# Optimization experiments

Hardware: AMD Instinct MI355X
Metric: run time of the kernel (lower is better)

The kernel has to match this reference:

```python
import jax, jax.numpy as jnp
import numpy as np

# Module config (matches init_kwargs)
C = 256          # in_channels
H = 8            # num_heads
T, L = 32, 16    # partition_size
S = T * L        # tokens per window = 512
B_ = 64          # number of windows
SCALE = H ** (-0.5)  # faithful to source: num_heads**-0.5


def setup_inputs() -> dict:
    key = jax.random.key(0)
    ks = jax.random.split(key, 6)
    x = jax.random.normal(ks[0], (B_, S, C), dtype=jnp.float32)
    # nn.Linear(C, 3C) weights: [out, in], bias: [out]
    qkv_w = jax.random.normal(ks[1], (3 * C, C), dtype=jnp.float32) * (1.0 / np.sqrt(C))
    qkv_b = jnp.zeros((3 * C,), dtype=jnp.float32)
    proj_w = jax.random.normal(ks[2], (C, C), dtype=jnp.float32) * (1.0 / np.sqrt(C))
    proj_b = jnp.zeros((C,), dtype=jnp.float32)
    # relative_position_bias_table for type_2: (2T-1, L, L, H), trunc_normal std=0.02 ~ small normal
    rel_table = jax.random.normal(ks[3], (2 * T - 1, L, L, H), dtype=jnp.float32) * 0.02
    return {"x": x, "qkv_w": qkv_w, "qkv_b": qkv_b,
            "proj_w": proj_w, "proj_b": proj_b, "rel_table": rel_table}


def _relative_position_bias(rel_table):
    # 1D relative index over T temporal positions, values in [0, 2T-2]
    idx = jnp.arange(T)[:, None] - jnp.arange(T)[None, :] + (T - 1)  # [T, T]
    b = rel_table[idx]                        # [T, T, L, L, H]
    b = b.transpose(0, 2, 1, 3, 4)            # [T, L, T, L, H]
    b = b.reshape(S, S, H)                    # [S, S, H]
    return b.transpose(2, 0, 1)[None]         # [1, H, S, S]


def reference(x, qkv_w, qkv_b, proj_w, proj_b, rel_table):
    Bw, Sw, Cw = x.shape
    d = Cw // H
    qkv = x @ qkv_w.T + qkv_b                              # [B_, S, 3C]
    qkv = qkv.reshape(Bw, Sw, 3, H, d).transpose(2, 0, 3, 1, 4)  # [3, B_, H, S, d]
    q, k, v = qkv[0], qkv[1], qkv[2]
    attn = jnp.einsum('bhsd,bhtd->bhst', q * SCALE, k)     # [B_, H, S, S]
    attn = attn + _relative_position_bias(rel_table)
    attn = jax.nn.softmax(attn, axis=-1)
    # attn_drop p=0.0 -> identity
    out = jnp.einsum('bhst,bhtd->bhsd', attn, v)           # [B_, H, S, d]
    out = out.transpose(0, 2, 1, 3).reshape(Bw, Sw, Cw)    # [B_, S, C]
    out = out @ proj_w.T + proj_b
    # proj_drop p=0.0 -> identity
    return out
```

## Files before the change

### kernel.cpp

```cpp
#include <hip/hip_runtime.h>
#include <stdint.h>

#define NB 64
#define NS 512
#define NC 256
#define NH 8
#define ND 32

typedef __attribute__((ext_vector_type(8))) short s8v;
typedef __attribute__((ext_vector_type(8))) unsigned short u8v;
typedef __attribute__((ext_vector_type(4))) float f4v;

#define LOG2E 1.4426950408889634f

static __device__ __forceinline__ uint16_t f2bf(float f) {
    uint32_t u = __builtin_bit_cast(uint32_t, f);
    u += 0x7fffu + ((u >> 16) & 1u);
    return (uint16_t)(u >> 16);
}
static __device__ __forceinline__ float bf2f(uint16_t h) {
    uint32_t u = ((uint32_t)h) << 16;
    return __builtin_bit_cast(float, u);
}
static __device__ __forceinline__ uint32_t cvtpk(float lo, float hi) {
    uint32_t r;
    asm("v_cvt_pk_bf16_f32 %0, %1, %2" : "=v"(r) : "v"(lo), "v"(hi));
    return r;
}

#if __has_builtin(__builtin_amdgcn_permlane32_swap)
static __device__ __forceinline__ void pl32(uint32_t& a, uint32_t& b) {
    auto r = __builtin_amdgcn_permlane32_swap(a, b, false, false);
    a = r[0]; b = r[1];
}
static __device__ __forceinline__ void pl16(uint32_t& a, uint32_t& b) {
    auto r = __builtin_amdgcn_permlane16_swap(a, b, false, false);
    a = r[0]; b = r[1];
}
#else
static __device__ __forceinline__ void pl32(uint32_t& a, uint32_t& b) {
    asm volatile("v_permlane32_swap_b32 %0, %1" : "+v"(a), "+v"(b));
}
static __device__ __forceinline__ void pl16(uint32_t& a, uint32_t& b) {
    asm volatile("v_permlane16_swap_b32 %0, %1" : "+v"(a), "+v"(b));
}
#endif

__global__ __launch_bounds__(256) void cvt_all(const float* __restrict__ x,
                                               const float* __restrict__ wq,
                                               const float* __restrict__ wp,
                                               uint16_t* __restrict__ xo,
                                               uint16_t* __restrict__ wqo,
                                               uint16_t* __restrict__ wpo) {
    int i = (blockIdx.x * 256 + threadIdx.x) * 8;
    const float* src; uint16_t* dst; int off;
    if (i < 8388608)      { src = x;  dst = xo;  off = i; }
    else if (i < 8585216) { src = wq; dst = wqo; off = i - 8388608; }
    else                  { src = wp; dst = wpo; off = i - 8585216; }
    f4v a = *(const f4v*)(src + off);
    f4v b = *(const f4v*)(src + off + 4);
    uint4 w;
    w.x = cvtpk(a[0], a[1]); w.y = cvtpk(a[2], a[3]);
    w.z = cvtpk(b[0], b[1]); w.w = cvtpk(b[2], b[3]);
    *(uint4*)(dst + off) = w;
}

__global__ __launch_bounds__(256) void rel_fill(const float* __restrict__ rel,
                                                uint16_t* __restrict__ rel2) {
    int id = blockIdx.x * 256 + threadIdx.x;
    int h = id / 20480, rem = id % 20480;
    int dt = rem / 320, q = rem % 320;
    int li = q / 20, lj = q % 20;
    float v = (lj < 16 && dt < 63) ? rel[(((dt << 4) + li) * 16 + lj) * 8 + h] * LOG2E : 0.f;
    rel2[id] = f2bf(v);
}

__global__ __launch_bounds__(256) void qkv_gemm(const uint16_t* __restrict__ X,
                                                const uint16_t* __restrict__ W,
                                                const float* __restrict__ Bv,
                                                uint16_t* __restrict__ Qo,
                                                uint16_t* __restrict__ Ko,
                                                uint16_t* __restrict__ Vo) {
    __shared__ uint16_t As[2][128 * 40];
    __shared__ uint16_t Bs[2][128 * 40];
    const int tid = threadIdx.x;
    const int bn = blockIdx.y * 128;
    const int bm = blockIdx.x * 128;
    const int lane = tid & 63, wv = tid >> 6;
    const int wm = (wv >> 1) * 64, wn = (wv & 1) * 64;
    const int lq = lane & 15, g = lane >> 4;
    const int srow = tid >> 1;
    const int scol = (tid & 1) * 16;

    const uint16_t* xs = X + (size_t)(bm + srow) * 256 + scol;
    const uint16_t* wsrc = W + (size_t)(bn + srow) * 256 + scol;

    f4v acc[4][4] = {};
    u8v xa, xb, wa, wb;

    xa = *(const u8v*)(xs);     xb = *(const u8v*)(xs + 8);
    wa = *(const u8v*)(wsrc);   wb = *(const u8v*)(wsrc + 8);
    *(u8v*)(&As[0][srow * 40 + scol])     = xa;
    *(u8v*)(&As[0][srow * 40 + scol + 8]) = xb;
    *(u8v*)(&Bs[0][srow * 40 + scol])     = wa;
    *(u8v*)(&Bs[0][srow * 40 + scol + 8]) = wb;
    __syncthreads();

    for (int ks = 0; ks < 8; ++ks) {
        const int cur = ks & 1;
        if (ks < 7) {
            const int k1 = (ks + 1) * 32;
            xa = *(const u8v*)(xs + k1);   xb = *(const u8v*)(xs + k1 + 8);
            wa = *(const u8v*)(wsrc + k1); wb = *(const u8v*)(wsrc + k1 + 8);
        }
        s8v af[4], bf[4];
        #pragma unroll
        for (int i = 0; i < 4; ++i) {
            af[i] = *(const s8v*)(&As[cur][(wm + i * 16 + lq) * 40 + g * 8]);
            bf[i] = *(const s8v*)(&Bs[cur][(wn + i * 16 + lq) * 40 + g * 8]);
        }
        #pragma unroll
        for (int mt = 0; mt < 4; ++mt)
            #pragma unroll
            for (int nt = 0; nt < 4; ++nt)
                acc[mt][nt] = __builtin_amdgcn_mfma_f32_16x16x32_bf16(af[mt], bf[nt], acc[mt][nt], 0, 0, 0);
        if (ks < 7) {
            *(u8v*)(&As[cur ^ 1][srow * 40 + scol])     = xa;
            *(u8v*)(&As[cur ^ 1][srow * 40 + scol + 8]) = xb;
            *(u8v*)(&Bs[cur ^ 1][srow * 40 + scol])     = wa;
            *(u8v*)(&Bs[cur ^ 1][srow * 40 + scol + 8]) = wb;
        }
        __syncthreads();
    }

    const int gsel = bn >> 8;
    const float scl = (gsel == 0) ? (0.35355339059327373f * LOG2E) : 1.0f;
    #pragma unroll
    for (int nt = 0; nt < 4; ++nt) {
        const int ng = bn + wn + nt * 16 + lq;
        const float bv = Bv[ng];
        const int c = ng & 255, hh = c >> 5, dd = c & 31;
        #pragma unroll
        for (int mt = 0; mt < 4; ++mt) {
            #pragma unroll
            for (int r = 0; r < 4; ++r) {
                const int m = bm + wm + mt * 16 + g * 4 + r;
                const int b = m >> 9, s = m & 511;
                const uint16_t val = f2bf((acc[mt][nt][r] + bv) * scl);
                if (gsel == 0)      Qo[((size_t)(b * 8 + hh) * 512 + s) * 32 + dd] = val;
                else if (gsel == 1) Ko[((size_t)(b * 8 + hh) * 512 + s) * 32 + dd] = val;
                else                Vo[((size_t)(b * 8 + hh) * 32 + dd) * 512 + s] = val;
            }
        }
    }
}

__global__ __launch_bounds__(512) void attn_kern(const uint16_t* __restrict__ Q,
                                                 const uint16_t* __restrict__ K,
                                                 const uint16_t* __restrict__ V,
                                                 const uint16_t* __restrict__ REL2,
                                                 uint16_t* __restrict__ AO) {
    __shared__ uint16_t Ks[64 * 40];
    __shared__ uint16_t Vs[32 * 80];
    __shared__ uint16_t Rel[64 * 320];

    const int p = blockIdx.x;
    const int h  = p & 7;
    const int qq = (p >> 3) & 3;
    const int b  = p >> 5;
    const int tid = threadIdx.x, lane = tid & 63, wv = tid >> 6;
    const int lq = lane & 15, g = lane >> 4;
    const int bh = b * 8 + h;
    const int qw = qq * 128 + wv * 16;
    const int ti = (qw >> 4);

    s8v qf = *(const s8v*)(Q + ((size_t)bh * 512 + qw + lq) * 32 + g * 8);
    const uint16_t* kg = K + (size_t)bh * 16384;
    const uint16_t* vg = V + (size_t)bh * 16384;

    {
        const uint16_t* rsrc = REL2 + (size_t)h * 20480;
        #pragma unroll
        for (int it = 0; it < 5; ++it) {
            int off = it * 4096 + tid * 8;
            *(u8v*)(Rel + off) = *(const u8v*)(rsrc + off);
        }
    }

    const bool isK = (tid < 256);
    const int t2 = tid & 255;
    const int ktrow = t2 >> 2, ktcol = (t2 & 3) * 8;
    const int vtrow = t2 >> 3, vtcol = (t2 & 7) * 8;
    const uint16_t* gsrc = isK ? (kg + (size_t)ktrow * 32 + ktcol)
                               : (vg + (size_t)vtrow * 512 + vtcol);
    uint16_t* ldst = isK ? (Ks + ktrow * 40 + ktcol)
                         : (Vs + vtrow * 80 + vtcol);
    const int gstep = isK ? (64 * 32) : 64;

    f4v o0 = {}, o1 = {};
    float mrow = -3.0e38f, lrow = 0.f;

    u8v sreg = *(const u8v*)(gsrc);

    for (int tile = 0; tile < 8; ++tile) {
        const int t0 = tile * 64;

        __syncthreads();
        *(u8v*)(ldst) = sreg;
        __syncthreads();

        if (tile < 7) {
            sreg = *(const u8v*)(gsrc + (size_t)(tile + 1) * gstep);
        }

        f4v a0, a1, a2, a3;
        {
            const int tj0 = t0 >> 4;
            const uint16_t* rb = Rel + lq * 20 + g * 4;
            ushort4 z0 = *(const ushort4*)(rb + (ti - tj0 - 0 + 31) * 320);
            ushort4 z1 = *(const ushort4*)(rb + (ti - tj0 - 1 + 31) * 320);
            ushort4 z2 = *(const ushort4*)(rb + (ti - tj0 - 2 + 31) * 320);
            ushort4 z3 = *(const ushort4*)(rb + (ti - tj0 - 3 + 31) * 320);
            a0[0]=bf2f(z0.x); a0[1]=bf2f(z0.y); a0[2]=bf2f(z0.z); a0[3]=bf2f(z0.w);
            a1[0]=bf2f(z1.x); a1[1]=bf2f(z1.y); a1[2]=bf2f(z1.z); a1[3]=bf2f(z1.w);
            a2[0]=bf2f(z2.x); a2[1]=bf2f(z2.y); a2[2]=bf2f(z2.z); a2[3]=bf2f(z2.w);
            a3[0]=bf2f(z3.x); a3[1]=bf2f(z3.y); a3[2]=bf2f(z3.z); a3[3]=bf2f(z3.w);
        }
        a0 = __builtin_amdgcn_mfma_f32_16x16x32_bf16(*(const s8v*)(Ks + ( 0 + lq) * 40 + g * 8), qf, a0, 0, 0, 0);
        a1 = __builtin_amdgcn_mfma_f32_16x16x32_bf16(*(const s8v*)(Ks + (16 + lq) * 40 + g * 8), qf, a1, 0, 0, 0);
        a2 = __builtin_amdgcn_mfma_f32_16x16x32_bf16(*(const s8v*)(Ks + (32 + lq) * 40 + g * 8), qf, a2, 0, 0, 0);
        a3 = __builtin_amdgcn_mfma_f32_16x16x32_bf16(*(const s8v*)(Ks + (48 + lq) * 40 + g * 8), qf, a3, 0, 0, 0);

        float p01 = fmaxf(fmaxf(a0[0], a0[1]), fmaxf(a0[2], a0[3]));
        float p23 = fmaxf(fmaxf(a1[0], a1[1]), fmaxf(a1[2], a1[3]));
        float p45 = fmaxf(fmaxf(a2[0], a2[1]), fmaxf(a2[2], a2[3]));
        float p67 = fmaxf(fmaxf(a3[0], a3[1]), fmaxf(a3[2], a3[3]));
        float pmax = fmaxf(fmaxf(p01, p23), fmaxf(p45, p67));
        pmax = fmaxf(pmax, __shfl_xor(pmax, 16));
        pmax = fmaxf(pmax, __shfl_xor(pmax, 32));

        if (!__all(pmax - mrow <= 8.0f)) {
            float mnew = fmaxf(mrow, pmax);
            float scale = __builtin_amdgcn_exp2f(mrow - mnew);
            lrow *= scale;
            float s0 = __shfl(scale, g * 4 + 0);
            float s1 = __shfl(scale, g * 4 + 1);
            float s2 = __shfl(scale, g * 4 + 2);
            float s3 = __shfl(scale, g * 4 + 3);
            o0[0] *= s0; o0[1] *= s1; o0[2] *= s2; o0[3] *= s3;
            o1[0] *= s0; o1[1] *= s1; o1[2] *= s2; o1[3] *= s3;
            mrow = mnew;
        }

        float lsum = 0.f;
        #pragma unroll
        for (int r = 0; r < 4; ++r) {
            a0[r] = __builtin_amdgcn_exp2f(a0[r] - mrow); lsum += a0[r];
            a1[r] = __builtin_amdgcn_exp2f(a1[r] - mrow); lsum += a1[r];
            a2[r] = __builtin_amdgcn_exp2f(a2[r] - mrow); lsum += a2[r];
            a3[r] = __builtin_amdgcn_exp2f(a3[r] - mrow); lsum += a3[r];
        }
        lrow += lsum;

        {
            uint32_t A0 = cvtpk(a0[0], a0[1]);
            uint32_t A1 = cvtpk(a0[2], a0[3]);
            uint32_t B0 = cvtpk(a1[0], a1[1]);
            uint32_t B1 = cvtpk(a1[2], a1[3]);
            pl32(A0, B0); pl16(A0, B0);
            pl32(A1, B1); pl16(A1, B1);
            uint4 wq; wq.x = A0; wq.y = A1; wq.z = B0; wq.w = B1;
            s8v pf = __builtin_bit_cast(s8v, wq);
            s8v vf0 = *(const s8v*)(Vs + lq * 80 + g * 8);
            s8v vf2 = *(const s8v*)(Vs + (lq + 16) * 80 + g * 8);
            o0 = __builtin_amdgcn_mfma_f32_16x16x32_bf16(pf, vf0, o0, 0, 0, 0);
            o1 = __builtin_amdgcn_mfma_f32_16x16x32_bf16(pf, vf2, o1, 0, 0, 0);
        }
        {
            uint32_t A0 = cvtpk(a2[0], a2[1]);
            uint32_t A1 = cvtpk(a2[2], a2[3]);
            uint32_t B0 = cvtpk(a3[0], a3[1]);
            uint32_t B1 = cvtpk(a3[2], a3[3]);
            pl32(A0, B0); pl16(A0, B0);
            pl32(A1, B1); pl16(A1, B1);
            uint4 wq; wq.x = A0; wq.y = A1; wq.z = B0; wq.w = B1;
            s8v pf = __builtin_bit_cast(s8v, wq);
            s8v vf1 = *(const s8v*)(Vs + lq * 80 + 32 + g * 8);
            s8v vf3 = *(const s8v*)(Vs + (lq + 16) * 80 + 32 + g * 8);
            o0 = __builtin_amdgcn_mfma_f32_16x16x32_bf16(pf, vf1, o0, 0, 0, 0);
            o1 = __builtin_amdgcn_mfma_f32_16x16x32_bf16(pf, vf3, o1, 0, 0, 0);
        }
    }

    lrow += __shfl_xor(lrow, 16);
    lrow += __shfl_xor(lrow, 32);
    const float inv = 1.0f / lrow;
    #pragma unroll
    for (int r = 0; r < 4; ++r) {
        const float iv = __shfl(inv, g * 4 + r);
        const int srow = b * 512 + qw + g * 4 + r;
        uint16_t* dst = AO + (size_t)srow * 256 + h * 32 + lq;
        dst[0]  = f2bf(o0[r] * iv);
        dst[16] = f2bf(o1[r] * iv);
    }
}

__global__ __launch_bounds__(256) void proj_gemm(const uint16_t* __restrict__ A,
                                                 const uint16_t* __restrict__ W,
                                                 const float* __restrict__ Bv,
                                                 float* __restrict__ Out) {
    __shared__ uint16_t As[2][128 * 40];
    __shared__ uint16_t Bs[2][128 * 40];
    const int tid = threadIdx.x;
    const int bn = blockIdx.y * 128;
    const int bm = blockIdx.x * 128;
    const int lane = tid & 63, wv = tid >> 6;
    const int wm = (wv >> 1) * 64, wn = (wv & 1) * 64;
    const int lq = lane & 15, g = lane >> 4;
    const int srow = tid >> 1;
    const int scol = (tid & 1) * 16;

    const uint16_t* as = A + (size_t)(bm + srow) * 256 + scol;
    const uint16_t* wsrc = W + (size_t)(bn + srow) * 256 + scol;

    f4v acc[4][4] = {};
    u8v xa, xb, wa, wb;

    xa = *(const u8v*)(as);     xb = *(const u8v*)(as + 8);
    wa = *(const u8v*)(wsrc);   wb = *(const u8v*)(wsrc + 8);
    *(u8v*)(&As[0][srow * 40 + scol])     = xa;
    *(u8v*)(&As[0][srow * 40 + scol + 8]) = xb;
    *(u8v*)(&Bs[0][srow * 40 + scol])     = wa;
    *(u8v*)(&Bs[0][srow * 40 + scol + 8]) = wb;
    __syncthreads();

    for (int ks = 0; ks < 8; ++ks) {
        const int cur = ks & 1;
        if (ks < 7) {
            const int k1 = (ks + 1) * 32;
            xa = *(const u8v*)(as + k1);   xb = *(const u8v*)(as + k1 + 8);
            wa = *(const u8v*)(wsrc + k1); wb = *(const u8v*)(wsrc + k1 + 8);
        }
        s8v af[4], bf[4];
        #pragma unroll
        for (int i = 0; i < 4; ++i) {
            af[i] = *(const s8v*)(&As[cur][(wm + i * 16 + lq) * 40 + g * 8]);
            bf[i] = *(const s8v*)(&Bs[cur][(wn + i * 16 + lq) * 40 + g * 8]);
        }
        #pragma unroll
        for (int mt = 0; mt < 4; ++mt)
            #pragma unroll
            for (int nt = 0; nt < 4; ++nt)
                acc[mt][nt] = __builtin_amdgcn_mfma_f32_16x16x32_bf16(af[mt], bf[nt], acc[mt][nt], 0, 0, 0);
        if (ks < 7) {
            *(u8v*)(&As[cur ^ 1][srow * 40 + scol])     = xa;
            *(u8v*)(&As[cur ^ 1][srow * 40 + scol + 8]) = xb;
            *(u8v*)(&Bs[cur ^ 1][srow * 40 + scol])     = wa;
            *(u8v*)(&Bs[cur ^ 1][srow * 40 + scol + 8]) = wb;
        }
        __syncthreads();
    }

    #pragma unroll
    for (int nt = 0; nt < 4; ++nt) {
        const int n = bn + wn + nt * 16 + lq;
        const float bv = Bv[n];
        #pragma unroll
        for (int mt = 0; mt < 4; ++mt) {
            #pragma unroll
            for (int r = 0; r < 4; ++r) {
                const int mm = bm + wm + mt * 16 + g * 4 + r;
                Out[(size_t)mm * 256 + n] = acc[mt][nt][r] + bv;
            }
        }
    }
}

extern "C" void kernel_launch(void* const* d_in, const int* in_sizes, int n_in,
                              void* d_out, int out_size, void* d_ws, size_t ws_size,
                              hipStream_t stream) {
    const float* x      = (const float*)d_in[0];
    const float* qkv_w  = (const float*)d_in[1];
    const float* qkv_b  = (const float*)d_in[2];
    const float* proj_w = (const float*)d_in[3];
    const float* proj_b = (const float*)d_in[4];
    const float* rel    = (const float*)d_in[5];
    float* out = (float*)d_out;

    uint16_t* ws = (uint16_t*)d_ws;
    const size_t QE = (size_t)NB * NH * NS * ND;
    uint16_t* Qb   = ws;
    uint16_t* Kb   = Qb + QE;
    uint16_t* Vb   = Kb + QE;
    uint16_t* Rb   = Vb + QE;
    uint16_t* REL2 = Rb + QE;
    uint16_t* Wqb  = REL2 + 163840;
    uint16_t* Wpb  = Wqb + 196608;

    cvt_all<<<4224, 256, 0, stream>>>(x, qkv_w, proj_w, Rb, Wqb, Wpb);
    rel_fill<<<640, 256, 0, stream>>>(rel, REL2);
    qkv_gemm<<<dim3(256, 6), 256, 0, stream>>>(Rb, Wqb, qkv_b, Qb, Kb, Vb);
    attn_kern<<<2048, 512, 0, stream>>>(Qb, Kb, Vb, REL2, Rb);
    proj_gemm<<<dim3(256, 2), 256, 0, stream>>>(Rb, Wpb, proj_b, out);
}
```

Before: 109.2 us.

## Fuse x fp32-to-bf16 conversion into QKV GEMM and vectorize V stores

Drops the separate conversion pass over x: the QKV GEMM now loads fp32 x directly and converts it to bf16 while staging tiles into shared memory. The conversion kernel now handles only the weights. This avoids writing and re-reading a bf16 copy of x, at the cost of each of the six column blocks re-reading fp32 x, which doubles its load bytes. Separately, the transposed V epilogue now uses permlane swaps to pack 8 consecutive sequence elements per lane into 16-byte stores instead of scattered 2-byte stores.

```diff
diff --git a/kernel.cpp b/kernel.cpp
--- a/kernel.cpp
+++ b/kernel.cpp
@@ -46,17 +46,14 @@
 }
 #endif
 
-__global__ __launch_bounds__(256) void cvt_all(const float* __restrict__ x,
-                                               const float* __restrict__ wq,
-                                               const float* __restrict__ wp,
-                                               uint16_t* __restrict__ xo,
-                                               uint16_t* __restrict__ wqo,
-                                               uint16_t* __restrict__ wpo) {
+__global__ __launch_bounds__(256) void cvt_w(const float* __restrict__ wq,
+                                             const float* __restrict__ wp,
+                                             uint16_t* __restrict__ wqo,
+                                             uint16_t* __restrict__ wpo) {
     int i = (blockIdx.x * 256 + threadIdx.x) * 8;
     const float* src; uint16_t* dst; int off;
-    if (i < 8388608)      { src = x;  dst = xo;  off = i; }
-    else if (i < 8585216) { src = wq; dst = wqo; off = i - 8388608; }
-    else                  { src = wp; dst = wpo; off = i - 8585216; }
+    if (i < 196608) { src = wq; dst = wqo; off = i; }
+    else            { src = wp; dst = wpo; off = i - 196608; }
     f4v a = *(const f4v*)(src + off);
     f4v b = *(const f4v*)(src + off + 4);
     uint4 w;
@@ -75,7 +72,7 @@
     rel2[id] = f2bf(v);
 }
 
-__global__ __launch_bounds__(256) void qkv_gemm(const uint16_t* __restrict__ X,
+__global__ __launch_bounds__(256) void qkv_gemm(const float* __restrict__ X,
                                                 const uint16_t* __restrict__ W,
                                                 const float* __restrict__ Bv,
                                                 uint16_t* __restrict__ Qo,
@@ -92,16 +89,25 @@
     const int srow = tid >> 1;
     const int scol = (tid & 1) * 16;
 
-    const uint16_t* xs = X + (size_t)(bm + srow) * 256 + scol;
+    const float* xs = X + (size_t)(bm + srow) * 256 + scol;
     const uint16_t* wsrc = W + (size_t)(bn + srow) * 256 + scol;
 
     f4v acc[4][4] = {};
-    u8v xa, xb, wa, wb;
-
-    xa = *(const u8v*)(xs);     xb = *(const u8v*)(xs + 8);
-    wa = *(const u8v*)(wsrc);   wb = *(const u8v*)(wsrc + 8);
-    *(u8v*)(&As[0][srow * 40 + scol])     = xa;
-    *(u8v*)(&As[0][srow * 40 + scol + 8]) = xb;
+    f4v x0, x1, x2, x3;
+    u8v wa, wb;
+
+    x0 = *(const f4v*)(xs);      x1 = *(const f4v*)(xs + 4);
+    x2 = *(const f4v*)(xs + 8);  x3 = *(const f4v*)(xs + 12);
+    wa = *(const u8v*)(wsrc);    wb = *(const u8v*)(wsrc + 8);
+    {
+        uint4 q0, q1;
+        q0.x = cvtpk(x0[0], x0[1]); q0.y = cvtpk(x0[2], x0[3]);
+        q0.z = cvtpk(x1[0], x1[1]); q0.w = cvtpk(x1[2], x1[3]);
+        q1.x = cvtpk(x2[0], x2[1]); q1.y = cvtpk(x2[2], x2[3]);
+        q1.z = cvtpk(x3[0], x3[1]); q1.w = cvtpk(x3[2], x3[3]);
+        *(uint4*)(&As[0][srow * 40 + scol])     = q0;
+        *(uint4*)(&As[0][srow * 40 + scol + 8]) = q1;
+    }
     *(u8v*)(&Bs[0][srow * 40 + scol])     = wa;
     *(u8v*)(&Bs[0][srow * 40 + scol + 8]) = wb;
     __syncthreads();
@@ -110,8 +116,9 @@
         const int cur = ks & 1;
         if (ks < 7) {
             const int k1 = (ks + 1) * 32;
-            xa = *(const u8v*)(xs + k1);   xb = *(const u8v*)(xs + k1 + 8);
-            wa = *(const u8v*)(wsrc + k1); wb = *(const u8v*)(wsrc + k1 + 8);
+            x0 = *(const f4v*)(xs + k1);      x1 = *(const f4v*)(xs + k1 + 4);
+            x2 = *(const f4v*)(xs + k1 + 8);  x3 = *(const f4v*)(xs + k1 + 12);
+            wa = *(const u8v*)(wsrc + k1);    wb = *(const u8v*)(wsrc + k1 + 8);
         }
         s8v af[4], bf[4];
         #pragma unroll
@@ -125,8 +132,13 @@
             for (int nt = 0; nt < 4; ++nt)
                 acc[mt][nt] = __builtin_amdgcn_mfma_f32_16x16x32_bf16(af[mt], bf[nt], acc[mt][nt], 0, 0, 0);
         if (ks < 7) {
-            *(u8v*)(&As[cur ^ 1][srow * 40 + scol])     = xa;
-            *(u8v*)(&As[cur ^ 1][srow * 40 + scol + 8]) = xb;
+            uint4 q0, q1;
+            q0.x = cvtpk(x0[0], x0[1]); q0.y = cvtpk(x0[2], x0[3]);
+            q0.z = cvtpk(x1[0], x1[1]); q0.w = cvtpk(x1[2], x1[3]);
+            q1.x = cvtpk(x2[0], x2[1]); q1.y = cvtpk(x2[2], x2[3]);
+            q1.z = cvtpk(x3[0], x3[1]); q1.w = cvtpk(x3[2], x3[3]);
+            *(uint4*)(&As[cur ^ 1][srow * 40 + scol])     = q0;
+            *(uint4*)(&As[cur ^ 1][srow * 40 + scol + 8]) = q1;
             *(u8v*)(&Bs[cur ^ 1][srow * 40 + scol])     = wa;
             *(u8v*)(&Bs[cur ^ 1][srow * 40 + scol + 8]) = wb;
         }
@@ -134,22 +146,45 @@
     }
 
     const int gsel = bn >> 8;
-    const float scl = (gsel == 0) ? (0.35355339059327373f * LOG2E) : 1.0f;
-    #pragma unroll
-    for (int nt = 0; nt < 4; ++nt) {
-        const int ng = bn + wn + nt * 16 + lq;
-        const float bv = Bv[ng];
-        const int c = ng & 255, hh = c >> 5, dd = c & 31;
-        #pragma unroll
-        for (int mt = 0; mt < 4; ++mt) {
+    if (gsel == 2) {
+        #pragma unroll
+        for (int nt = 0; nt < 4; ++nt) {
+            const int ng = bn + wn + nt * 16 + lq;
+            const float bv = Bv[ng];
+            const int c = ng & 255, hh = c >> 5, dd = c & 31;
             #pragma unroll
-            for (int r = 0; r < 4; ++r) {
-                const int m = bm + wm + mt * 16 + g * 4 + r;
-                const int b = m >> 9, s = m & 511;
-                const uint16_t val = f2bf((acc[mt][nt][r] + bv) * scl);
-                if (gsel == 0)      Qo[((size_t)(b * 8 + hh) * 512 + s) * 32 + dd] = val;
-                else if (gsel == 1) Ko[((size_t)(b * 8 + hh) * 512 + s) * 32 + dd] = val;
-                else                Vo[((size_t)(b * 8 + hh) * 32 + dd) * 512 + s] = val;
+            for (int mtp = 0; mtp < 2; ++mtp) {
+                f4v u = acc[mtp * 2][nt], v = acc[mtp * 2 + 1][nt];
+                uint32_t A0 = cvtpk(u[0] + bv, u[1] + bv);
+                uint32_t A1 = cvtpk(u[2] + bv, u[3] + bv);
+                uint32_t B0 = cvtpk(v[0] + bv, v[1] + bv);
+                uint32_t B1 = cvtpk(v[2] + bv, v[3] + bv);
+                pl32(A0, B0); pl16(A0, B0);
+                pl32(A1, B1); pl16(A1, B1);
+                uint4 wq; wq.x = A0; wq.y = A1; wq.z = B0; wq.w = B1;
+                const int m0 = bm + wm + mtp * 32;
+                const int b = m0 >> 9;
+                const int s0 = (m0 & 511) + g * 8;
+                *(uint4*)(Vo + ((size_t)(b * 8 + hh) * 32 + dd) * 512 + s0) = wq;
+            }
+        }
+    } else {
+        const float scl = (gsel == 0) ? (0.35355339059327373f * LOG2E) : 1.0f;
+        #pragma unroll
+        for (int nt = 0; nt < 4; ++nt) {
+            const int ng = bn + wn + nt * 16 + lq;
+            const float bv = Bv[ng];
+            const int c = ng & 255, hh = c >> 5, dd = c & 31;
+            #pragma unroll
+            for (int mt = 0; mt < 4; ++mt) {
+                #pragma unroll
+                for (int r = 0; r < 4; ++r) {
+                    const int m = bm + wm + mt * 16 + g * 4 + r;
+                    const int b = m >> 9, s = m & 511;
+                    const uint16_t val = f2bf((acc[mt][nt][r] + bv) * scl);
+                    if (gsel == 0) Qo[((size_t)(b * 8 + hh) * 512 + s) * 32 + dd] = val;
+                    else           Ko[((size_t)(b * 8 + hh) * 512 + s) * 32 + dd] = val;
+                }
             }
         }
     }
@@ -397,9 +432,9 @@
     uint16_t* Wqb  = REL2 + 163840;
     uint16_t* Wpb  = Wqb + 196608;
 
-    cvt_all<<<4224, 256, 0, stream>>>(x, qkv_w, proj_w, Rb, Wqb, Wpb);
+    cvt_w<<<128, 256, 0, stream>>>(qkv_w, proj_w, Wqb, Wpb);
     rel_fill<<<640, 256, 0, stream>>>(rel, REL2);
-    qkv_gemm<<<dim3(256, 6), 256, 0, stream>>>(Rb, Wqb, qkv_b, Qb, Kb, Vb);
+    qkv_gemm<<<dim3(256, 6), 256, 0, stream>>>(x, Wqb, qkv_b, Qb, Kb, Vb);
     attn_kern<<<2048, 512, 0, stream>>>(Qb, Kb, Vb, REL2, Rb);
     proj_gemm<<<dim3(256, 2), 256, 0, stream>>>(Rb, Wpb, proj_b, out);
 }
```

Result: faster. 103.9 us (-4.9%).
